# Performance work log

Hardware: AMD Instinct MI355X
Metric: run time of the kernel (lower is better)

## Reference

```python
import jax, jax.numpy as jnp
import numpy as np

D_MODEL = 192; D_INNER = 384; N_STATE = 16; D_CONV = 4; DT_RANK = 12; DEPTH = 24
PATCH = 16; STRIDE = 16; IMG = 128; EPS = 1e-5


def _ln(x, w, b):
    m = jnp.mean(x, -1, keepdims=True)
    v = jnp.mean((x - m) ** 2, -1, keepdims=True)
    return (x - m) * jax.lax.rsqrt(v + EPS) * w + b


def _mamba_dir(xz, cw, cb, xpw, dpw, dpb, Alog, Dv):
    # xz: (B, L, 2*d_inner); one direction of the bidirectional Mamba mixer
    xp, z = jnp.split(xz, 2, axis=-1)               # (B,L,di) each
    xc = jnp.transpose(xp, (0, 2, 1))               # (B,di,L)
    xc = jnp.pad(xc, ((0, 0), (0, 0), (D_CONV - 1, 0)))  # causal pad
    xc = jax.lax.conv_general_dilated(
        xc, cw, (1,), 'VALID',
        dimension_numbers=('NCH', 'OIH', 'NCH'),
        feature_group_count=D_INNER) + cb[None, :, None]
    u = jax.nn.silu(jnp.transpose(xc, (0, 2, 1)))   # (B,L,di)
    dbl = u @ xpw.T                                  # (B,L,dt_rank+2N)
    dt, Bm, Cm = jnp.split(dbl, [DT_RANK, DT_RANK + N_STATE], axis=-1)
    dt = jax.nn.softplus(dt @ dpw.T + dpb)           # (B,L,di)
    A = -jnp.exp(Alog)                               # (di,N)
    dA = jnp.exp(dt[..., None] * A)                  # (B,L,di,N)
    dBu = (dt * u)[..., None] * Bm[:, :, None, :]    # (B,L,di,N)

    def comb(c1, c2):
        a1, b1 = c1
        a2, b2 = c2
        return a1 * a2, a2 * b1 + b2

    _, h = jax.lax.associative_scan(comb, (dA, dBu), axis=1)
    y = jnp.einsum('bldn,bln->bld', h, Cm) + u * Dv
    return y * jax.nn.silu(z)


def _forward(x, patch_w, patch_b, ln_w, ln_b, in_w,
             cf_w, cf_b, xpf_w, dtf_w, dtf_b, Alog_f, D_f,
             cbk_w, cbk_b, xpb_w, dtb_w, dtb_b, Alog_b, D_b,
             out_w, nf_w, nf_b, head_w, head_b):
    B = x.shape[0]
    p = jax.lax.conv_general_dilated(
        x, patch_w, (STRIDE,) * 3, 'VALID',
        dimension_numbers=('NCDHW', 'OIDHW', 'NCDHW')) + patch_b[None, :, None, None, None]
    hidden = p.reshape(B, D_MODEL, -1).transpose(0, 2, 1)  # (B, L=512, D)
    residual = jnp.zeros_like(hidden)

    xs = (ln_w, ln_b, in_w, cf_w, cf_b, xpf_w, dtf_w, dtf_b, Alog_f, D_f,
          cbk_w, cbk_b, xpb_w, dtb_w, dtb_b, Alog_b, D_b, out_w)

    def step(carry, pl):
        hidden, residual = carry
        (lw, lb, iw, cfw, cfb, xpf, dwf, dbf, Af, Dfv,
         cbw, cbb, xpb, dwb, dbb, Ab, Dbv, ow) = pl
        residual = residual + hidden
        hn = _ln(residual, lw, lb)
        xz = hn @ iw.T                               # (B,L,2di)
        yf = _mamba_dir(xz, cfw, cfb, xpf, dwf, dbf, Af, Dfv)
        yb = jnp.flip(_mamba_dir(jnp.flip(xz, 1), cbw, cbb, xpb, dwb, dbb, Ab, Dbv), 1)
        hidden = (yf + yb) @ ow.T
        return (hidden, residual), None

    (hidden, residual), _ = jax.lax.scan(step, (hidden, residual), xs)
    final = _ln(residual + hidden, nf_w, nf_b)
    feat = final[:, -1, :]                           # final_pool_type='none' -> last token
    return feat @ head_w.T + head_b


def setup_inputs() -> dict:
    key = jax.random.key(0)
    ks = jax.random.split(key, 16)
    rn = lambda k, s, sc=0.02: jax.random.normal(k, s, jnp.float32) * sc
    d = {}
    d['x'] = jax.random.normal(ks[0], (1, 1, IMG, IMG, IMG), jnp.float32)
    d['patch_w'] = rn(ks[1], (D_MODEL, 1, PATCH, PATCH, PATCH), 0.05)
    d['patch_b'] = jnp.zeros((D_MODEL,), jnp.float32)
    d['ln_w'] = jnp.ones((DEPTH, D_MODEL), jnp.float32)
    d['ln_b'] = jnp.zeros((DEPTH, D_MODEL), jnp.float32)
    d['in_w'] = rn(ks[2], (DEPTH, 2 * D_INNER, D_MODEL))
    d['cf_w'] = rn(ks[3], (DEPTH, D_INNER, 1, D_CONV), 0.2)
    d['cf_b'] = jnp.zeros((DEPTH, D_INNER), jnp.float32)
    d['xpf_w'] = rn(ks[4], (DEPTH, DT_RANK + 2 * N_STATE, D_INNER))
    d['dtf_w'] = rn(ks[5], (DEPTH, D_INNER, DT_RANK), 0.1)
    d['dtf_b'] = jnp.full((DEPTH, D_INNER), -4.6, jnp.float32)  # softplus -> dt~0.01
    d['Alog_f'] = jnp.log(jnp.broadcast_to(jnp.arange(1, N_STATE + 1, dtype=jnp.float32), (DEPTH, D_INNER, N_STATE)))
    d['D_f'] = jnp.ones((DEPTH, D_INNER), jnp.float32)
    d['cbk_w'] = rn(ks[6], (DEPTH, D_INNER, 1, D_CONV), 0.2)
    d['cbk_b'] = jnp.zeros((DEPTH, D_INNER), jnp.float32)
    d['xpb_w'] = rn(ks[7], (DEPTH, DT_RANK + 2 * N_STATE, D_INNER))
    d['dtb_w'] = rn(ks[8], (DEPTH, D_INNER, DT_RANK), 0.1)
    d['dtb_b'] = jnp.full((DEPTH, D_INNER), -4.6, jnp.float32)
    d['Alog_b'] = jnp.log(jnp.broadcast_to(jnp.arange(1, N_STATE + 1, dtype=jnp.float32), (DEPTH, D_INNER, N_STATE)))
    d['D_b'] = jnp.ones((DEPTH, D_INNER), jnp.float32)
    d['out_w'] = rn(ks[9], (DEPTH, D_MODEL, D_INNER))
    d['nf_w'] = jnp.ones((D_MODEL,), jnp.float32)
    d['nf_b'] = jnp.zeros((D_MODEL,), jnp.float32)
    d['head_w'] = rn(ks[10], (2, D_MODEL))
    d['head_b'] = jnp.zeros((2,), jnp.float32)
    return d


def reference(x, patch_w, patch_b, ln_w, ln_b, in_w,
              cf_w, cf_b, xpf_w, dtf_w, dtf_b, Alog_f, D_f,
              cbk_w, cbk_b, xpb_w, dtb_w, dtb_b, Alog_b, D_b,
              out_w, nf_w, nf_b, head_w, head_b):
    return _forward(x, patch_w, patch_b, ln_w, ln_b, in_w,
                    cf_w, cf_b, xpf_w, dtf_w, dtf_b, Alog_f, D_f,
                    cbk_w, cbk_b, xpb_w, dtb_w, dtb_b, Alog_b, D_b,
                    out_w, nf_w, nf_b, head_w, head_b)
```

## Files before the change

kernel.cpp:

```cpp
#include <hip/hip_runtime.h>
#include <hip/hip_bf16.h>

#define D_MODEL 192
#define D_INNER 384
#define N_STATE 16
#define DT_RANK 12
#define DEPTH 24
#define SEQ 512
#define NCHUNK 8
#define CLEN 64
#define TS 68
#define AS 33
#define PART_STRIDE (SEQ * D_MODEL)
#define USTR (SEQ * D_INNER)
#define KSPLIT 16
#define NBLK 512

typedef __hip_bfloat16 bf16;
typedef unsigned short u16;

__device__ __forceinline__ float silu_f(float x) { return x / (1.f + __expf(-x)); }
__device__ __forceinline__ float softplus_f(float x) {
    return (x > 20.f) ? x : log1pf(__expf(x));
}
__device__ __forceinline__ float bf2f(unsigned u) {
    return __uint_as_float(u << 16);
}
__device__ __forceinline__ u16 f2bu(float f) {
    bf16 b = __float2bfloat16(f);
    return *reinterpret_cast<u16*>(&b);
}

__device__ __forceinline__ float aload(const float* p) {
    return __hip_atomic_load(p, __ATOMIC_RELAXED, __HIP_MEMORY_SCOPE_AGENT);
}
__device__ __forceinline__ void astore(float* p, float v) {
    __hip_atomic_store(p, v, __ATOMIC_RELAXED, __HIP_MEMORY_SCOPE_AGENT);
}
__device__ __forceinline__ float4 aload4(const float* p) {
    return make_float4(aload(p), aload(p + 1), aload(p + 2), aload(p + 3));
}
__device__ __forceinline__ void astore4(float* p, float4 v) {
    astore(p, v.x); astore(p + 1, v.y); astore(p + 2, v.z); astore(p + 3, v.w);
}

template<typename T> __device__ __forceinline__ float ld(const void* p, long i) {
    return ((const float*)p)[i];
}
template<> __device__ __forceinline__ float ld<bf16>(const void* p, long i) {
    return bf2f(((const u16*)p)[i]);
}
template<typename T> __device__ __forceinline__ float4 ld4(const void* p, long i) {
    return *(const float4*)((const float*)p + i);
}
template<> __device__ __forceinline__ float4 ld4<bf16>(const void* p, long i) {
    const ushort4 v = *(const ushort4*)((const u16*)p + i);
    return make_float4(bf2f(v.x), bf2f(v.y), bf2f(v.z), bf2f(v.w));
}
template<typename T> __device__ __forceinline__ void st(void* p, int i, float v) {
    ((float*)p)[i] = v;
}
template<> __device__ __forceinline__ void st<bf16>(void* p, int i, float v) {
    ((bf16*)p)[i] = __float2bfloat16(v);
}
__device__ __forceinline__ float dot4(const float4& a, const float4& b) {
    return a.x * b.x + a.y * b.y + a.z * b.z + a.w * b.w;
}
__device__ __forceinline__ void ld8b(const u16* p, float4& a, float4& b) {
    const uint4 u = *(const uint4*)p;
    a.x = bf2f(u.x & 0xffffu); a.y = bf2f(u.x >> 16);
    a.z = bf2f(u.y & 0xffffu); a.w = bf2f(u.y >> 16);
    b.x = bf2f(u.z & 0xffffu); b.y = bf2f(u.z >> 16);
    b.z = bf2f(u.w & 0xffffu); b.w = bf2f(u.w >> 16);
}
__device__ __forceinline__ float4 ld4b(const u16* p) {
    const uint2 u = *(const uint2*)p;
    return make_float4(bf2f(u.x & 0xffffu), bf2f(u.x >> 16),
                       bf2f(u.y & 0xffffu), bf2f(u.y >> 16));
}

__device__ __forceinline__ void gbar_full(unsigned* flags, unsigned* gen, unsigned target) {
    __syncthreads();
    const int bid = blockIdx.x, tid = threadIdx.x;
    if (tid == 0) {
        __threadfence();
        __hip_atomic_store(&flags[bid], target, __ATOMIC_RELAXED, __HIP_MEMORY_SCOPE_AGENT);
    }
    if (bid == 0) {
        int spins = 0;
        for (;;) {
            const unsigned va = __hip_atomic_load(&flags[tid], __ATOMIC_RELAXED, __HIP_MEMORY_SCOPE_AGENT);
            const unsigned vb = __hip_atomic_load(&flags[tid + 256], __ATOMIC_RELAXED, __HIP_MEMORY_SCOPE_AGENT);
            const bool ok = (va >= target) && (vb >= target);
            if (__syncthreads_and(ok)) break;
            if (++spins > (1 << 20)) break;
            __builtin_amdgcn_s_sleep(1);
        }
        if (tid == 0)
            __hip_atomic_store(gen, target, __ATOMIC_RELAXED, __HIP_MEMORY_SCOPE_AGENT);
    } else if (tid == 0) {
        int spins = 0;
        while (__hip_atomic_load(gen, __ATOMIC_RELAXED, __HIP_MEMORY_SCOPE_AGENT) < target) {
            if (++spins > (1 << 20)) break;
            __builtin_amdgcn_s_sleep(1);
        }
    }
    if (tid == 0) __threadfence();
    __syncthreads();
}

__device__ __forceinline__ void gbar_lite(unsigned* flags, unsigned* gen, unsigned target) {
    asm volatile("s_waitcnt vmcnt(0)" ::: "memory");
    __syncthreads();
    const int bid = blockIdx.x, tid = threadIdx.x;
    if (tid == 0)
        __hip_atomic_store(&flags[bid], target, __ATOMIC_RELAXED, __HIP_MEMORY_SCOPE_AGENT);
    if (bid == 0) {
        int spins = 0;
        for (;;) {
            const unsigned va = __hip_atomic_load(&flags[tid], __ATOMIC_RELAXED, __HIP_MEMORY_SCOPE_AGENT);
            const unsigned vb = __hip_atomic_load(&flags[tid + 256], __ATOMIC_RELAXED, __HIP_MEMORY_SCOPE_AGENT);
            const bool ok = (va >= target) && (vb >= target);
            if (__syncthreads_and(ok)) break;
            if (++spins > (1 << 20)) break;
            __builtin_amdgcn_s_sleep(1);
        }
        if (tid == 0)
            __hip_atomic_store(gen, target, __ATOMIC_RELAXED, __HIP_MEMORY_SCOPE_AGENT);
    } else if (tid == 0) {
        int spins = 0;
        while (__hip_atomic_load(gen, __ATOMIC_RELAXED, __HIP_MEMORY_SCOPE_AGENT) < target) {
            if (++spins > (1 << 20)) break;
            __builtin_amdgcn_s_sleep(1);
        }
    }
    __syncthreads();
}

__device__ void cvtB(const void* s, u16* d, long n, long g, long str, int isb) {
    if (isb) {
        const u16* p = (const u16*)s;
        for (long i = g * 4; i < n; i += str * 4) *(ushort4*)(d + i) = *(const ushort4*)(p + i);
    } else {
        const float* p = (const float*)s;
        for (long i = g * 4; i < n; i += str * 4) {
            const float4 v = *(const float4*)(p + i);
            ushort4 o; o.x = f2bu(v.x); o.y = f2bu(v.y); o.z = f2bu(v.z); o.w = f2bu(v.w);
            *(ushort4*)(d + i) = o;
        }
    }
}
__device__ void cvtF(const void* s, float* d, long n, long g, long str, int isb) {
    if (isb) {
        const u16* p = (const u16*)s;
        for (long i = g * 4; i < n; i += str * 4) {
            const ushort4 v = *(const ushort4*)(p + i);
            *(float4*)(d + i) = make_float4(bf2f(v.x), bf2f(v.y), bf2f(v.z), bf2f(v.w));
        }
    } else {
        const float* p = (const float*)s;
        for (long i = g * 4; i < n; i += str * 4) *(float4*)(d + i) = *(const float4*)(p + i);
    }
}
__device__ void cvtNA(const void* s, float* d, long n, long g, long str, int isb) {
    if (isb) {
        const u16* p = (const u16*)s;
        for (long i = g * 4; i < n; i += str * 4) {
            const ushort4 v = *(const ushort4*)(p + i);
            *(float4*)(d + i) = make_float4(-__expf(bf2f(v.x)), -__expf(bf2f(v.y)),
                                            -__expf(bf2f(v.z)), -__expf(bf2f(v.w)));
        }
    } else {
        const float* p = (const float*)s;
        for (long i = g * 4; i < n; i += str * 4) {
            const float4 v = *(const float4*)(p + i);
            *(float4*)(d + i) = make_float4(-__expf(v.x), -__expf(v.y), -__expf(v.z), -__expf(v.w));
        }
    }
}

template<typename T>
__device__ void final_phase(int tid, const float* res, const float* y, const void* ow,
                            const void* nw, const void* nb, const void* hw, const void* hb,
                            void* out, float* syf, float* f, float* red) {
    for (int i = tid; i < D_INNER; i += 256)
        syf[i] = aload(&y[(long)511 * D_INNER + i]) + aload(&y[(long)USTR + 511 * D_INNER + i]);
    __syncthreads();
    float v = 0.f;
    if (tid < D_MODEL) {
        float acc = 0.f;
        const long wrow = (long)(DEPTH - 1) * D_MODEL * D_INNER + (long)tid * D_INNER;
        for (int k = 0; k < D_INNER; k += 4)
            acc += dot4(ld4<T>(ow, wrow + k), *(const float4*)&syf[k]);
        v = aload(&res[511 * D_MODEL + tid]) + acc;
    }
    float s = v;
    #pragma unroll
    for (int o = 32; o > 0; o >>= 1) s += __shfl_down(s, o, 64);
    if ((tid & 63) == 0 && tid < D_MODEL) red[tid >> 6] = s;
    __syncthreads();
    const float mean = (red[0] + red[1] + red[2]) * (1.f / D_MODEL);
    const float d = (tid < D_MODEL) ? (v - mean) : 0.f;
    float s2 = d * d;
    #pragma unroll
    for (int o = 32; o > 0; o >>= 1) s2 += __shfl_down(s2, o, 64);
    if ((tid & 63) == 0 && tid < D_MODEL) red[3 + (tid >> 6)] = s2;
    __syncthreads();
    const float var = (red[3] + red[4] + red[5]) * (1.f / D_MODEL);
    if (tid < D_MODEL)
        f[tid] = d * rsqrtf(var + 1e-5f) * ld<T>(nw, tid) + ld<T>(nb, tid);
    __syncthreads();
    if (tid < 2) {
        float a2 = ld<T>(hb, tid);
        for (int c = 0; c < D_MODEL; ++c) a2 += f[c] * ld<T>(hw, tid * D_MODEL + c);
        st<T>(out, tid, a2);
    }
}

struct MegaArgs {
    const void *x, *pw, *pb, *lnw, *lnb, *inw, *cfw, *cfb, *xpfw, *dtfw, *dtfb, *Af, *Dfv;
    const void *cbw, *cbb, *xpbw, *dtbw, *dtbb, *Ab, *Dbv, *ow, *nfw, *nfb, *hw, *hb;
    void* out;
    unsigned* bar;
    float *hidC, *res0, *res1, *xz, *u, *dbl, *dt, *y, *chunkH, *chunkP;
    float *lnwF, *lnbF, *cbfF, *cbbF, *dtbfF, *dtbbF, *negAfF, *negAbF, *DfF, *DbF, *pbF;
    u16 *inwB, *owB, *xB, *pwB, *xpwfB, *xpwbB, *dtwfB, *dtwbB, *cwfB, *cwbB;
};

__global__ void init_kernel(unsigned* bar) {
    for (int i = threadIdx.x; i < 1024; i += 256) bar[i] = 0;
}

__global__ void __launch_bounds__(256, 2) mega_kernel(MegaArgs a) {
    __shared__ float smem[6144];
    const int bid = blockIdx.x;
    const int tid = threadIdx.x;
    unsigned* bflags = a.bar;
    unsigned* bgen = a.bar + 576;
    unsigned gen_ctr = 0;
    const int isb = (((const unsigned*)a.lnw)[0] != 0x3F800000u);

    {
        const long g = (long)bid * 256 + tid;
        const long str = (long)NBLK * 256;
        cvtB(a.inw,  a.inwB,  3538944, g, str, isb);
        cvtB(a.ow,   a.owB,   1769472, g, str, isb);
        cvtB(a.x,    a.xB,    2097152, g, str, isb);
        cvtB(a.pw,   a.pwB,    786432, g, str, isb);
        cvtB(a.xpfw, a.xpwfB,  405504, g, str, isb);
        cvtB(a.xpbw, a.xpwbB,  405504, g, str, isb);
        cvtB(a.dtfw, a.dtwfB,  110592, g, str, isb);
        cvtB(a.dtbw, a.dtwbB,  110592, g, str, isb);
        cvtB(a.cfw,  a.cwfB,    36864, g, str, isb);
        cvtB(a.cbw,  a.cwbB,    36864, g, str, isb);
        cvtF(a.lnw,  a.lnwF,     4608, g, str, isb);
        cvtF(a.lnb,  a.lnbF,     4608, g, str, isb);
        cvtF(a.cfb,  a.cbfF,     9216, g, str, isb);
        cvtF(a.cbb,  a.cbbF,     9216, g, str, isb);
        cvtF(a.dtfb, a.dtbfF,    9216, g, str, isb);
        cvtF(a.dtbb, a.dtbbF,    9216, g, str, isb);
        cvtF(a.pb,   a.pbF,       192, g, str, isb);
        cvtNA(a.Af,  a.negAfF,  147456, g, str, isb);
        cvtNA(a.Ab,  a.negAbF,  147456, g, str, isb);
        cvtF(a.Dfv,  a.DfF,      9216, g, str, isb);
        cvtF(a.Dbv,  a.DbF,      9216, g, str, isb);
    }
    gbar_full(bflags, bgen, ++gen_ctr);

    {
        float* As_ = smem;
        float* Ws  = smem + 1056;
        const int ty = tid >> 4, tx = tid & 15;
        for (int unit = bid; unit < 768; unit += NBLK) {
            const int mt = unit & 15, nt = (unit >> 4) % 3, ks = unit / 48;
            const int m0 = mt * 32, n0 = nt * 64, kk0 = ks * 256;
            float acc[2][4] = {};
            for (int kk = kk0; kk < kk0 + 256; kk += 32) {
                for (int e = tid; e < 1024; e += 256) {
                    const int m = e >> 5, k = e & 31;
                    const int kid = kk + k, t = m0 + m;
                    const int dz = kid >> 8, dy = (kid >> 4) & 15, dx = kid & 15;
                    const int pz = t >> 6, py = (t >> 3) & 7, px = t & 7;
                    As_[k * AS + m] = bf2f(a.xB[(long)(pz * 16 + dz) * 16384 + (py * 16 + dy) * 128 + (px * 16 + dx)]);
                }
                for (int e = tid; e < 2048; e += 256) {
                    const int n = e >> 5, k = e & 31;
                    Ws[k * TS + n] = bf2f(a.pwB[(long)(n0 + n) * 4096 + kk + k]);
                }
                __syncthreads();
                #pragma unroll 8
                for (int k = 0; k < 32; ++k) {
                    const float a0 = As_[k * AS + ty * 2];
                    const float a1 = As_[k * AS + ty * 2 + 1];
                    const float4 w4 = *(const float4*)&Ws[k * TS + tx * 4];
                    acc[0][0] += a0 * w4.x; acc[0][1] += a0 * w4.y;
                    acc[0][2] += a0 * w4.z; acc[0][3] += a0 * w4.w;
                    acc[1][0] += a1 * w4.x; acc[1][1] += a1 * w4.y;
                    acc[1][2] += a1 * w4.z; acc[1][3] += a1 * w4.w;
                }
                __syncthreads();
            }
            float* C = a.hidC + (long)ks * PART_STRIDE;
            #pragma unroll
            for (int i = 0; i < 2; ++i) {
                float4 o4 = make_float4(acc[i][0], acc[i][1], acc[i][2], acc[i][3]);
                if (ks == 0) {
                    o4.x += a.pbF[n0 + tx * 4 + 0];
                    o4.y += a.pbF[n0 + tx * 4 + 1];
                    o4.z += a.pbF[n0 + tx * 4 + 2];
                    o4.w += a.pbF[n0 + tx * 4 + 3];
                }
                astore4(&C[(m0 + ty * 2 + i) * D_MODEL + n0 + tx * 4], o4);
            }
        }
    }
    gbar_lite(bflags, bgen, ++gen_ctr);

    const int ch = tid >> 4, np = tid & 15;
    float* sU  = smem;
    float* sDT = smem + 1024;
    float* sBC = smem + 2048;
    float* sZ  = smem + 4096;
    float* sY  = smem + 5120;
    int dg = 0, chunk = 0, dir2 = 0;
    float Areg = 0.f, Dval = 0.f;

    for (int l = 0; l < DEPTH; ++l) {
        const int first = (l == 0);
        const float* resIn = (l & 1) ? a.res1 : a.res0;
        float* resOut      = (l & 1) ? a.res0 : a.res1;

        if (bid < 256) {
            float* sy  = smem;
            float* lnS = smem + 768;
            float* hnS = smem + 1152;
            const int t0 = bid * 2;
            if (!first) {
                for (int i = tid; i < 2 * D_INNER; i += 256) {
                    const int tt = i / D_INNER, d = i - tt * D_INNER;
                    const long o = (long)(t0 + tt) * D_INNER + d;
                    sy[i] = aload(&a.y[o]) + aload(&a.y[(long)USTR + o]);
                }
            }
            __syncthreads();
            if (tid < D_MODEL) {
                float accB[2];
                if (first) {
                    #pragma unroll
                    for (int tt = 0; tt < 2; ++tt) {
                        float s = 0.f;
                        #pragma unroll
                        for (int sp = 0; sp < KSPLIT; ++sp)
                            s += aload(&a.hidC[(long)sp * PART_STRIDE + (t0 + tt) * D_MODEL + tid]);
                        accB[tt] = s;
                    }
                } else {
                    accB[0] = accB[1] = 0.f;
                    const u16* wr = a.owB + (long)(l - 1) * D_MODEL * D_INNER + (long)tid * D_INNER;
                    for (int k = 0; k < D_INNER; k += 8) {
                        float4 va, vb;
                        ld8b(wr + k, va, vb);
                        accB[0] += dot4(va, *(const float4*)&sy[k]) + dot4(vb, *(const float4*)&sy[k + 4]);
                        accB[1] += dot4(va, *(const float4*)&sy[D_INNER + k]) + dot4(vb, *(const float4*)&sy[D_INNER + k + 4]);
                    }
                }
                #pragma unroll
                for (int tt = 0; tt < 2; ++tt) {
                    const float rv = accB[tt] + (first ? 0.f : aload(&resIn[(t0 + tt) * D_MODEL + tid]));
                    lnS[tt * D_MODEL + tid] = rv;
                    astore(&resOut[(t0 + tt) * D_MODEL + tid], rv);
                }
            }
            __syncthreads();
            {
                const int w = tid >> 6, lane = tid & 63;
                if (w < 2) {
                    const float v0 = lnS[w * D_MODEL + lane];
                    const float v1 = lnS[w * D_MODEL + lane + 64];
                    const float v2 = lnS[w * D_MODEL + lane + 128];
                    float s = v0 + v1 + v2;
                    #pragma unroll
                    for (int o = 32; o > 0; o >>= 1) s += __shfl_xor(s, o, 64);
                    const float mean = s * (1.f / D_MODEL);
                    const float d0 = v0 - mean, d1 = v1 - mean, d2 = v2 - mean;
                    float s2 = d0 * d0 + d1 * d1 + d2 * d2;
                    #pragma unroll
                    for (int o = 32; o > 0; o >>= 1) s2 += __shfl_xor(s2, o, 64);
                    const float rstd = rsqrtf(s2 * (1.f / D_MODEL) + 1e-5f);
                    hnS[w * D_MODEL + lane]       = d0 * rstd * a.lnwF[l * D_MODEL + lane]       + a.lnbF[l * D_MODEL + lane];
                    hnS[w * D_MODEL + lane + 64]  = d1 * rstd * a.lnwF[l * D_MODEL + lane + 64]  + a.lnbF[l * D_MODEL + lane + 64];
                    hnS[w * D_MODEL + lane + 128] = d2 * rstd * a.lnwF[l * D_MODEL + lane + 128] + a.lnbF[l * D_MODEL + lane + 128];
                }
            }
            __syncthreads();
            float accD[3][2] = {};
            const u16* w0 = a.inwB + (long)l * 2 * D_INNER * D_MODEL;
            for (int k = 0; k < D_MODEL; k += 8) {
                #pragma unroll
                for (int r = 0; r < 3; ++r) {
                    float4 va, vb;
                    ld8b(w0 + (long)(tid + r * 256) * D_MODEL + k, va, vb);
                    #pragma unroll
                    for (int tt = 0; tt < 2; ++tt) {
                        accD[r][tt] += dot4(va, *(const float4*)&hnS[tt * D_MODEL + k])
                                     + dot4(vb, *(const float4*)&hnS[tt * D_MODEL + k + 4]);
                    }
                }
            }
            #pragma unroll
            for (int r = 0; r < 3; ++r)
                #pragma unroll
                for (int tt = 0; tt < 2; ++tt)
                    astore(&a.xz[(long)(t0 + tt) * 2 * D_INNER + tid + r * 256], accD[r][tt]);
        }
        gbar_lite(bflags, bgen, ++gen_ctr);

        {
            float* su   = smem;
            float* dblP = smem + 768;
            float* dblS = smem + 960;
            const int dir = bid >> 8;
            const u16* cwB   = dir ? a.cwbB  : a.cwfB;
            const float* cbF = dir ? a.cbbF  : a.cbfF;
            const u16* xpwB  = dir ? a.xpwbB : a.xpwfB;
            const u16* dtwB  = dir ? a.dtwbB : a.dtwfB;
            const float* dtbF = dir ? a.dtbbF : a.dtbfF;
            const int t0 = (bid & 255) * 2;
            float* ub = a.u + (long)dir * USTR;
            for (int i = tid; i < 2 * D_INNER; i += 256) {
                const int tt = i / D_INNER, d = i - tt * D_INNER;
                const int t = t0 + tt;
                const float4 w4 = ld4b(cwB + (long)(l * D_INNER + d) * 4);
                const float cwk[4] = {w4.x, w4.y, w4.z, w4.w};
                float acc = cbF[l * D_INNER + d];
                #pragma unroll
                for (int k = 0; k < 4; ++k) {
                    const int ii = t + k - 3;
                    if (ii >= 0) {
                        const int src = dir ? (511 - ii) : ii;
                        acc += aload(&a.xz[(long)src * 2 * D_INNER + d]) * cwk[k];
                    }
                }
                const float uv = silu_f(acc);
                su[tt * D_INNER + d] = uv;
                astore(&ub[(long)t * D_INNER + d], uv);
            }
            __syncthreads();
            if (tid < 176) {
                const int half = tid / 88;
                const int r = tid - half * 88;
                const int tt = r / 44, out = r - tt * 44;
                const u16* wr = xpwB + (long)(l * 44 + out) * D_INNER;
                const int k0 = half * 192;
                float acc = 0.f;
                for (int k = k0; k < k0 + 192; k += 8) {
                    float4 va, vb;
                    ld8b(wr + k, va, vb);
                    acc += dot4(va, *(const float4*)&su[tt * D_INNER + k])
                         + dot4(vb, *(const float4*)&su[tt * D_INNER + k + 4]);
                }
                dblP[half * 96 + tt * 48 + out] = acc;
            }
            __syncthreads();
            if (tid < 88) {
                const int tt = tid / 44, out = tid - tt * 44;
                const float s = dblP[tt * 48 + out] + dblP[96 + tt * 48 + out];
                dblS[tt * 48 + out] = s;
                astore(&a.dbl[(long)dir * SEQ * 44 + (long)(t0 + tt) * 44 + out], s);
            }
            __syncthreads();
            float* dtp = a.dt + (long)dir * USTR;
            for (int i = tid; i < 2 * D_INNER; i += 256) {
                const int tt = i / D_INNER, d = i - tt * D_INNER;
                const u16* wr = dtwB + (long)(l * D_INNER + d) * DT_RANK;
                const float4 wa = ld4b(wr), wb2 = ld4b(wr + 4), wc = ld4b(wr + 8);
                const float* ds = &dblS[tt * 48];
                float acc = dtbF[l * D_INNER + d]
                    + wa.x * ds[0] + wa.y * ds[1] + wa.z * ds[2] + wa.w * ds[3]
                    + wb2.x * ds[4] + wb2.y * ds[5] + wb2.z * ds[6] + wb2.w * ds[7]
                    + wc.x * ds[8] + wc.y * ds[9] + wc.z * ds[10] + wc.w * ds[11];
                astore(&dtp[(long)(t0 + tt) * D_INNER + d], softplus_f(acc));
            }
        }
        gbar_lite(bflags, bgen, ++gen_ctr);

        if (bid < 384) {
            dg = bid % 24; chunk = (bid / 24) & 7; dir2 = bid / 192;
            const int d0 = dg * 16, d = d0 + ch;
            const int t0s = chunk * CLEN;
            const float* ub  = a.u  + (long)dir2 * USTR;
            const float* dtp = a.dt + (long)dir2 * USTR;
            const float* db  = a.dbl + (long)dir2 * SEQ * 44;
            {
                const int t = tid >> 2, dl4 = (tid & 3) * 4;
                const int tg = t0s + t;
                const long base = (long)tg * D_INNER + d0 + dl4;
                *(float4*)&sU[t * 16 + dl4]  = aload4(&ub[base]);
                *(float4*)&sDT[t * 16 + dl4] = aload4(&dtp[base]);
                const int out_l = dir2 ? (511 - tg) : tg;
                *(float4*)&sZ[t * 16 + dl4] = aload4(&a.xz[(long)out_l * 2 * D_INNER + D_INNER + d0 + dl4]);
            }
            for (int i = tid; i < 512; i += 256) {
                const int t = i >> 3, j4 = (i & 7) * 4;
                *(float4*)&sBC[t * 32 + j4] = aload4(&db[(long)(t0s + t) * 44 + DT_RANK + j4]);
            }
            const float* negA = dir2 ? a.negAbF : a.negAfF;
            Areg = negA[(long)(l * D_INNER + d) * N_STATE + np];
            Dval = (dir2 ? a.DbF : a.DfF)[l * D_INNER + d];
            __syncthreads();
            float h = 0.f, dts = 0.f;
            for (int t = 0; t < CLEN; ++t) {
                const float dtv = sDT[t * 16 + ch];
                h = __expf(dtv * Areg) * h + (dtv * sU[t * 16 + ch]) * sBC[t * 32 + np];
                dts += dtv;
            }
            const long cb = ((long)(dir2 * NCHUNK + chunk) * D_INNER + d) * N_STATE + np;
            astore(&a.chunkH[cb], h);
            astore(&a.chunkP[cb], __expf(Areg * dts));
        }
        gbar_lite(bflags, bgen, ++gen_ctr);

        if (bid < 384) {
            const int d0 = dg * 16, d = d0 + ch;
            const int t0s = chunk * CLEN;
            float hs[NCHUNK - 1], ps[NCHUNK - 1];
            #pragma unroll
            for (int c = 0; c < NCHUNK - 1; ++c) {
                if (c < chunk) {
                    const long cb = ((long)(dir2 * NCHUNK + c) * D_INNER + d) * N_STATE + np;
                    hs[c] = aload(&a.chunkH[cb]);
                    ps[c] = aload(&a.chunkP[cb]);
                }
            }
            float h = 0.f;
            #pragma unroll
            for (int c = 0; c < NCHUNK - 1; ++c)
                if (c < chunk) h = ps[c] * h + hs[c];
            for (int t = 0; t < CLEN; ++t) {
                const float dtv = sDT[t * 16 + ch];
                const float uv = sU[t * 16 + ch];
                h = __expf(dtv * Areg) * h + (dtv * uv) * sBC[t * 32 + np];
                float part = h * sBC[t * 32 + 16 + np];
                part += __shfl_xor(part, 1, 64);
                part += __shfl_xor(part, 2, 64);
                part += __shfl_xor(part, 4, 64);
                part += __shfl_xor(part, 8, 64);
                if (np == 0)
                    sY[t * 16 + ch] = (part + uv * Dval) * silu_f(sZ[t * 16 + ch]);
            }
            __syncthreads();
            {
                const int t = tid >> 2, dl4 = (tid & 3) * 4;
                const int tg = t0s + t;
                const int out_l = dir2 ? (511 - tg) : tg;
                float* yb = a.y + (long)dir2 * USTR;
                astore4(&yb[(long)out_l * D_INNER + d0 + dl4], *(float4*)&sY[t * 16 + dl4]);
            }
        }
        gbar_lite(bflags, bgen, ++gen_ctr);
    }

    if (bid == 0) {
        float* syf = smem;
        float* f   = smem + 384;
        float* red = smem + 576;
        if (isb) final_phase<bf16>(tid, a.res0, a.y, a.ow, a.nfw, a.nfb, a.hw, a.hb, a.out, syf, f, red);
        else     final_phase<float>(tid, a.res0, a.y, a.ow, a.nfw, a.nfb, a.hw, a.hb, a.out, syf, f, red);
    }
}

extern "C" void kernel_launch(void* const* d_in, const int* in_sizes, int n_in,
                              void* d_out, int out_size, void* d_ws, size_t ws_size,
                              hipStream_t stream) {
    (void)in_sizes; (void)n_in; (void)out_size; (void)ws_size;
    const void* x    = d_in[0];
    const void* pw   = d_in[1];
    const void* pb   = d_in[2];
    const void* lnw  = d_in[3];
    const void* lnb  = d_in[4];
    const void* inw  = d_in[5];
    const void* cfw  = d_in[6];
    const void* cfb  = d_in[7];
    const void* xpfw = d_in[8];
    const void* dtfw = d_in[9];
    const void* dtfb = d_in[10];
    const void* Af   = d_in[11];
    const void* Dfv  = d_in[12];
    const void* cbw  = d_in[13];
    const void* cbb  = d_in[14];
    const void* xpbw = d_in[15];
    const void* dtbw = d_in[16];
    const void* dtbb = d_in[17];
    const void* Ab   = d_in[18];
    const void* Dbv  = d_in[19];
    const void* ow   = d_in[20];
    const void* nfw  = d_in[21];
    const void* nfb  = d_in[22];
    const void* hw   = d_in[23];
    const void* hb   = d_in[24];

    unsigned* bar = (unsigned*)d_ws;
    float* w = (float*)((char*)d_ws + 4096);
    float* hidC   = w;  w += KSPLIT * PART_STRIDE;
    float* res0   = w;  w += PART_STRIDE;
    float* res1   = w;  w += PART_STRIDE;
    float* xz     = w;  w += SEQ * 2 * D_INNER;
    float* u      = w;  w += 2 * USTR;
    float* dbl    = w;  w += 2 * SEQ * 44;
    float* dt     = w;  w += 2 * USTR;
    float* y      = w;  w += 2 * USTR;
    float* chunkH = w;  w += 2 * NCHUNK * D_INNER * N_STATE;
    float* chunkP = w;  w += 2 * NCHUNK * D_INNER * N_STATE;
    float* lnwF = w;  w += 4608;
    float* lnbF = w;  w += 4608;
    float* cbfF = w;  w += 9216;
    float* cbbF = w;  w += 9216;
    float* dtbfF = w; w += 9216;
    float* dtbbF = w; w += 9216;
    float* negAfF = w; w += 147456;
    float* negAbF = w; w += 147456;
    float* DfF = w;   w += 9216;
    float* DbF = w;   w += 9216;
    float* pbF = w;   w += 192;
    u16* b = (u16*)w;
    u16* inwB  = b;  b += 3538944;
    u16* owB   = b;  b += 1769472;
    u16* xB    = b;  b += 2097152;
    u16* pwB   = b;  b += 786432;
    u16* xpwfB = b;  b += 405504;
    u16* xpwbB = b;  b += 405504;
    u16* dtwfB = b;  b += 110592;
    u16* dtwbB = b;  b += 110592;
    u16* cwfB  = b;  b += 36864;
    u16* cwbB  = b;  b += 36864;

    MegaArgs ma;
    ma.x = x; ma.pw = pw; ma.pb = pb; ma.lnw = lnw; ma.lnb = lnb; ma.inw = inw;
    ma.cfw = cfw; ma.cfb = cfb; ma.xpfw = xpfw; ma.dtfw = dtfw; ma.dtfb = dtfb;
    ma.Af = Af; ma.Dfv = Dfv; ma.cbw = cbw; ma.cbb = cbb; ma.xpbw = xpbw;
    ma.dtbw = dtbw; ma.dtbb = dtbb; ma.Ab = Ab; ma.Dbv = Dbv; ma.ow = ow;
    ma.nfw = nfw; ma.nfb = nfb; ma.hw = hw; ma.hb = hb; ma.out = d_out;
    ma.bar = bar;
    ma.hidC = hidC; ma.res0 = res0; ma.res1 = res1; ma.xz = xz; ma.u = u;
    ma.dbl = dbl; ma.dt = dt; ma.y = y; ma.chunkH = chunkH; ma.chunkP = chunkP;
    ma.lnwF = lnwF; ma.lnbF = lnbF; ma.cbfF = cbfF; ma.cbbF = cbbF;
    ma.dtbfF = dtbfF; ma.dtbbF = dtbbF; ma.negAfF = negAfF; ma.negAbF = negAbF;
    ma.DfF = DfF; ma.DbF = DbF; ma.pbF = pbF;
    ma.inwB = inwB; ma.owB = owB; ma.xB = xB; ma.pwB = pwB;
    ma.xpwfB = xpwfB; ma.xpwbB = xpwbB; ma.dtwfB = dtwfB; ma.dtwbB = dtwbB;
    ma.cwfB = cwfB; ma.cwbB = cwbB;

    init_kernel<<<1, 256, 0, stream>>>(bar);
    mega_kernel<<<NBLK, 256, 0, stream>>>(ma);
}
```

Baseline: 2.123 ms.

## Pad barrier flags, tree-broadcast release, and replace scan barrier with per-chunk flags

The grid barrier now gives each block's flag its own padded slot, so flags no longer share cache lines. Release goes through a two-level fan-out: 16 relay blocks copy the generation and the other blocks poll their own relay slot instead of all spinning on one word. The global barrier between the chunk-local scan and the carry-in pass is replaced by per-chunk ready flags, so each chunk waits only on the earlier chunks it depends on. Atomic loads and stores are widened to 64-bit pairs, and the conv and dt-projection loops handle two channels per thread to halve the number of memory operations. The trade-offs are a larger workspace, more bookkeeping, and dependence on relaxed 64-bit atomics and spin flags for correctness.

```diff
diff --git a/kernel.cpp b/kernel.cpp
--- a/kernel.cpp
+++ b/kernel.cpp
@@ -15,9 +15,11 @@
 #define USTR (SEQ * D_INNER)
 #define KSPLIT 16
 #define NBLK 512
+#define FSTR 32
 
 typedef __hip_bfloat16 bf16;
 typedef unsigned short u16;
+typedef unsigned long long u64;
 
 __device__ __forceinline__ float silu_f(float x) { return x / (1.f + __expf(-x)); }
 __device__ __forceinline__ float softplus_f(float x) {
@@ -37,11 +39,26 @@
 __device__ __forceinline__ void astore(float* p, float v) {
     __hip_atomic_store(p, v, __ATOMIC_RELAXED, __HIP_MEMORY_SCOPE_AGENT);
 }
-__device__ __forceinline__ float4 aload4(const float* p) {
-    return make_float4(aload(p), aload(p + 1), aload(p + 2), aload(p + 3));
-}
-__device__ __forceinline__ void astore4(float* p, float4 v) {
-    astore(p, v.x); astore(p + 1, v.y); astore(p + 2, v.z); astore(p + 3, v.w);
+__device__ __forceinline__ unsigned aloadu(const unsigned* p) {
+    return __hip_atomic_load(p, __ATOMIC_RELAXED, __HIP_MEMORY_SCOPE_AGENT);
+}
+__device__ __forceinline__ void astoreu(unsigned* p, unsigned v) {
+    __hip_atomic_store(p, v, __ATOMIC_RELAXED, __HIP_MEMORY_SCOPE_AGENT);
+}
+__device__ __forceinline__ float2 aload2(const float* p) {
+    const u64 v = __hip_atomic_load((const u64*)p, __ATOMIC_RELAXED, __HIP_MEMORY_SCOPE_AGENT);
+    return make_float2(__uint_as_float((unsigned)v), __uint_as_float((unsigned)(v >> 32)));
+}
+__device__ __forceinline__ void astore2(float* p, float x, float y) {
+    const u64 v = (u64)__float_as_uint(x) | ((u64)__float_as_uint(y) << 32);
+    __hip_atomic_store((u64*)p, v, __ATOMIC_RELAXED, __HIP_MEMORY_SCOPE_AGENT);
+}
+__device__ __forceinline__ float4 aload4v(const float* p) {
+    const float2 a = aload2(p), b = aload2(p + 2);
+    return make_float4(a.x, a.y, b.x, b.y);
+}
+__device__ __forceinline__ void astore4v(float* p, float4 v) {
+    astore2(p, v.x, v.y); astore2(p + 2, v.z, v.w);
 }
 
 template<typename T> __device__ __forceinline__ float ld(const void* p, long i) {
@@ -79,61 +96,48 @@
                        bf2f(u.y & 0xffffu), bf2f(u.y >> 16));
 }
 
-__device__ __forceinline__ void gbar_full(unsigned* flags, unsigned* gen, unsigned target) {
+__device__ __forceinline__ void gbar(unsigned* bar, unsigned target, bool fence) {
+    asm volatile("s_waitcnt vmcnt(0)" ::: "memory");
     __syncthreads();
     const int bid = blockIdx.x, tid = threadIdx.x;
+    unsigned* gen0 = bar + 512 * FSTR;
     if (tid == 0) {
-        __threadfence();
-        __hip_atomic_store(&flags[bid], target, __ATOMIC_RELAXED, __HIP_MEMORY_SCOPE_AGENT);
+        if (fence) __threadfence();
+        astoreu(&bar[bid * FSTR], target);
     }
     if (bid == 0) {
         int spins = 0;
         for (;;) {
-            const unsigned va = __hip_atomic_load(&flags[tid], __ATOMIC_RELAXED, __HIP_MEMORY_SCOPE_AGENT);
-            const unsigned vb = __hip_atomic_load(&flags[tid + 256], __ATOMIC_RELAXED, __HIP_MEMORY_SCOPE_AGENT);
+            const unsigned va = aloadu(&bar[tid * FSTR]);
+            const unsigned vb = aloadu(&bar[(tid + 256) * FSTR]);
             const bool ok = (va >= target) && (vb >= target);
             if (__syncthreads_and(ok)) break;
             if (++spins > (1 << 20)) break;
             __builtin_amdgcn_s_sleep(1);
         }
-        if (tid == 0)
-            __hip_atomic_store(gen, target, __ATOMIC_RELAXED, __HIP_MEMORY_SCOPE_AGENT);
+        if (tid == 0) astoreu(gen0, target);
     } else if (tid == 0) {
         int spins = 0;
-        while (__hip_atomic_load(gen, __ATOMIC_RELAXED, __HIP_MEMORY_SCOPE_AGENT) < target) {
-            if (++spins > (1 << 20)) break;
-            __builtin_amdgcn_s_sleep(1);
-        }
-    }
-    if (tid == 0) __threadfence();
-    __syncthreads();
-}
-
-__device__ __forceinline__ void gbar_lite(unsigned* flags, unsigned* gen, unsigned target) {
-    asm volatile("s_waitcnt vmcnt(0)" ::: "memory");
-    __syncthreads();
-    const int bid = blockIdx.x, tid = threadIdx.x;
-    if (tid == 0)
-        __hip_atomic_store(&flags[bid], target, __ATOMIC_RELAXED, __HIP_MEMORY_SCOPE_AGENT);
-    if (bid == 0) {
-        int spins = 0;
-        for (;;) {
-            const unsigned va = __hip_atomic_load(&flags[tid], __ATOMIC_RELAXED, __HIP_MEMORY_SCOPE_AGENT);
-            const unsigned vb = __hip_atomic_load(&flags[tid + 256], __ATOMIC_RELAXED, __HIP_MEMORY_SCOPE_AGENT);
-            const bool ok = (va >= target) && (vb >= target);
-            if (__syncthreads_and(ok)) break;
-            if (++spins > (1 << 20)) break;
-            __builtin_amdgcn_s_sleep(1);
-        }
-        if (tid == 0)
-            __hip_atomic_store(gen, target, __ATOMIC_RELAXED, __HIP_MEMORY_SCOPE_AGENT);
-    } else if (tid == 0) {
-        int spins = 0;
-        while (__hip_atomic_load(gen, __ATOMIC_RELAXED, __HIP_MEMORY_SCOPE_AGENT) < target) {
-            if (++spins > (1 << 20)) break;
-            __builtin_amdgcn_s_sleep(1);
-        }
-    }
+        if (bid < 16) {
+            while (aloadu(gen0) < target) {
+                if (++spins > (1 << 20)) break;
+                __builtin_amdgcn_s_sleep(2);
+            }
+            astoreu(&gen0[bid * FSTR], target);
+        } else if (bid < 32) {
+            while (aloadu(gen0) < target) {
+                if (++spins > (1 << 20)) break;
+                __builtin_amdgcn_s_sleep(2);
+            }
+        } else {
+            unsigned* rl = &gen0[(bid >> 5) * FSTR];
+            while (aloadu(rl) < target) {
+                if (++spins > (1 << 20)) break;
+                __builtin_amdgcn_s_sleep(2);
+            }
+        }
+    }
+    if (fence && tid == 0) __threadfence();
     __syncthreads();
 }
 
@@ -228,15 +232,16 @@
 };
 
 __global__ void init_kernel(unsigned* bar) {
-    for (int i = threadIdx.x; i < 1024; i += 256) bar[i] = 0;
+    const int i = blockIdx.x * 256 + threadIdx.x;
+    ((uint4*)bar)[i] = make_uint4(0, 0, 0, 0);
 }
 
 __global__ void __launch_bounds__(256, 2) mega_kernel(MegaArgs a) {
     __shared__ float smem[6144];
     const int bid = blockIdx.x;
     const int tid = threadIdx.x;
-    unsigned* bflags = a.bar;
-    unsigned* bgen = a.bar + 576;
+    unsigned* bar = a.bar;
+    unsigned* scanR = a.bar + 528 * FSTR;
     unsigned gen_ctr = 0;
     const int isb = (((const unsigned*)a.lnw)[0] != 0x3F800000u);
 
@@ -265,7 +270,7 @@
         cvtF(a.Dfv,  a.DfF,      9216, g, str, isb);
         cvtF(a.Dbv,  a.DbF,      9216, g, str, isb);
     }
-    gbar_full(bflags, bgen, ++gen_ctr);
+    gbar(bar, ++gen_ctr, true);
 
     {
         float* As_ = smem;
@@ -310,11 +315,11 @@
                     o4.z += a.pbF[n0 + tx * 4 + 2];
                     o4.w += a.pbF[n0 + tx * 4 + 3];
                 }
-                astore4(&C[(m0 + ty * 2 + i) * D_MODEL + n0 + tx * 4], o4);
-            }
-        }
-    }
-    gbar_lite(bflags, bgen, ++gen_ctr);
+                astore4v(&C[(m0 + ty * 2 + i) * D_MODEL + n0 + tx * 4], o4);
+            }
+        }
+    }
+    gbar(bar, ++gen_ctr, false);
 
     const int ch = tid >> 4, np = tid & 15;
     float* sU  = smem;
@@ -322,8 +327,6 @@
     float* sBC = smem + 2048;
     float* sZ  = smem + 4096;
     float* sY  = smem + 5120;
-    int dg = 0, chunk = 0, dir2 = 0;
-    float Areg = 0.f, Dval = 0.f;
 
     for (int l = 0; l < DEPTH; ++l) {
         const int first = (l == 0);
@@ -336,10 +339,13 @@
             float* hnS = smem + 1152;
             const int t0 = bid * 2;
             if (!first) {
-                for (int i = tid; i < 2 * D_INNER; i += 256) {
-                    const int tt = i / D_INNER, d = i - tt * D_INNER;
-                    const long o = (long)(t0 + tt) * D_INNER + d;
-                    sy[i] = aload(&a.y[o]) + aload(&a.y[(long)USTR + o]);
+                for (int j = tid; j < 384; j += 256) {
+                    const int tt = j / 192, d2 = (j - tt * 192) * 2;
+                    const long o = (long)(t0 + tt) * D_INNER + d2;
+                    const float2 v1 = aload2(&a.y[o]);
+                    const float2 v2 = aload2(&a.y[(long)USTR + o]);
+                    sy[tt * D_INNER + d2]     = v1.x + v2.x;
+                    sy[tt * D_INNER + d2 + 1] = v1.y + v2.y;
                 }
             }
             __syncthreads();
@@ -413,7 +419,7 @@
                 for (int tt = 0; tt < 2; ++tt)
                     astore(&a.xz[(long)(t0 + tt) * 2 * D_INNER + tid + r * 256], accD[r][tt]);
         }
-        gbar_lite(bflags, bgen, ++gen_ctr);
+        gbar(bar, ++gen_ctr, false);
 
         {
             float* su   = smem;
@@ -427,23 +433,29 @@
             const float* dtbF = dir ? a.dtbbF : a.dtbfF;
             const int t0 = (bid & 255) * 2;
             float* ub = a.u + (long)dir * USTR;
-            for (int i = tid; i < 2 * D_INNER; i += 256) {
-                const int tt = i / D_INNER, d = i - tt * D_INNER;
+            for (int j = tid; j < 384; j += 256) {
+                const int tt = j / 192, d2 = (j - tt * 192) * 2;
                 const int t = t0 + tt;
-                const float4 w4 = ld4b(cwB + (long)(l * D_INNER + d) * 4);
-                const float cwk[4] = {w4.x, w4.y, w4.z, w4.w};
-                float acc = cbF[l * D_INNER + d];
+                float4 wa, wb;
+                ld8b(cwB + (long)(l * D_INNER + d2) * 4, wa, wb);
+                const float cw0[4] = {wa.x, wa.y, wa.z, wa.w};
+                const float cw1[4] = {wb.x, wb.y, wb.z, wb.w};
+                float acc0 = cbF[l * D_INNER + d2];
+                float acc1 = cbF[l * D_INNER + d2 + 1];
                 #pragma unroll
                 for (int k = 0; k < 4; ++k) {
                     const int ii = t + k - 3;
                     if (ii >= 0) {
                         const int src = dir ? (511 - ii) : ii;
-                        acc += aload(&a.xz[(long)src * 2 * D_INNER + d]) * cwk[k];
+                        const float2 xv = aload2(&a.xz[(long)src * 2 * D_INNER + d2]);
+                        acc0 += xv.x * cw0[k];
+                        acc1 += xv.y * cw1[k];
                     }
                 }
-                const float uv = silu_f(acc);
-                su[tt * D_INNER + d] = uv;
-                astore(&ub[(long)t * D_INNER + d], uv);
+                const float u0 = silu_f(acc0), u1 = silu_f(acc1);
+                su[tt * D_INNER + d2] = u0;
+                su[tt * D_INNER + d2 + 1] = u1;
+                astore2(&ub[(long)t * D_INNER + d2], u0, u1);
             }
             __syncthreads();
             if (tid < 176) {
@@ -470,22 +482,29 @@
             }
             __syncthreads();
             float* dtp = a.dt + (long)dir * USTR;
-            for (int i = tid; i < 2 * D_INNER; i += 256) {
-                const int tt = i / D_INNER, d = i - tt * D_INNER;
-                const u16* wr = dtwB + (long)(l * D_INNER + d) * DT_RANK;
-                const float4 wa = ld4b(wr), wb2 = ld4b(wr + 4), wc = ld4b(wr + 8);
+            for (int j = tid; j < 384; j += 256) {
+                const int tt = j / 192, d2 = (j - tt * 192) * 2;
+                const u16* wr = dtwB + (long)(l * D_INNER + d2) * DT_RANK;
+                float4 A0, B0; ld8b(wr, A0, B0);
+                const float4 C0 = ld4b(wr + 8);
+                float4 A1, B1; ld8b(wr + 12, A1, B1);
+                const float4 C1 = ld4b(wr + 20);
                 const float* ds = &dblS[tt * 48];
-                float acc = dtbF[l * D_INNER + d]
-                    + wa.x * ds[0] + wa.y * ds[1] + wa.z * ds[2] + wa.w * ds[3]
-                    + wb2.x * ds[4] + wb2.y * ds[5] + wb2.z * ds[6] + wb2.w * ds[7]
-                    + wc.x * ds[8] + wc.y * ds[9] + wc.z * ds[10] + wc.w * ds[11];
-                astore(&dtp[(long)(t0 + tt) * D_INNER + d], softplus_f(acc));
-            }
-        }
-        gbar_lite(bflags, bgen, ++gen_ctr);
+                const float4 ds0 = *(const float4*)ds;
+                const float4 ds1 = *(const float4*)(ds + 4);
+                const float4 ds2 = *(const float4*)(ds + 8);
+                const float acc0 = dtbF[l * D_INNER + d2]
+                    + dot4(A0, ds0) + dot4(B0, ds1) + dot4(C0, ds2);
+                const float acc1 = dtbF[l * D_INNER + d2 + 1]
+                    + dot4(A1, ds0) + dot4(B1, ds1) + dot4(C1, ds2);
+                astore2(&dtp[(long)(t0 + tt) * D_INNER + d2],
+                        softplus_f(acc0), softplus_f(acc1));
+            }
+        }
+        gbar(bar, ++gen_ctr, false);
 
         if (bid < 384) {
-            dg = bid % 24; chunk = (bid / 24) & 7; dir2 = bid / 192;
+            const int dg = bid % 24, chunk = (bid / 24) & 7, dir2 = bid / 192;
             const int d0 = dg * 16, d = d0 + ch;
             const int t0s = chunk * CLEN;
             const float* ub  = a.u  + (long)dir2 * USTR;
@@ -495,18 +514,18 @@
                 const int t = tid >> 2, dl4 = (tid & 3) * 4;
                 const int tg = t0s + t;
                 const long base = (long)tg * D_INNER + d0 + dl4;
-                *(float4*)&sU[t * 16 + dl4]  = aload4(&ub[base]);
-                *(float4*)&sDT[t * 16 + dl4] = aload4(&dtp[base]);
+                *(float4*)&sU[t * 16 + dl4]  = aload4v(&ub[base]);
+                *(float4*)&sDT[t * 16 + dl4] = aload4v(&dtp[base]);
                 const int out_l = dir2 ? (511 - tg) : tg;
-                *(float4*)&sZ[t * 16 + dl4] = aload4(&a.xz[(long)out_l * 2 * D_INNER + D_INNER + d0 + dl4]);
+                *(float4*)&sZ[t * 16 + dl4] = aload4v(&a.xz[(long)out_l * 2 * D_INNER + D_INNER + d0 + dl4]);
             }
             for (int i = tid; i < 512; i += 256) {
                 const int t = i >> 3, j4 = (i & 7) * 4;
-                *(float4*)&sBC[t * 32 + j4] = aload4(&db[(long)(t0s + t) * 44 + DT_RANK + j4]);
+                *(float4*)&sBC[t * 32 + j4] = aload4v(&db[(long)(t0s + t) * 44 + DT_RANK + j4]);
             }
             const float* negA = dir2 ? a.negAbF : a.negAfF;
-            Areg = negA[(long)(l * D_INNER + d) * N_STATE + np];
-            Dval = (dir2 ? a.DbF : a.DfF)[l * D_INNER + d];
+            const float Areg = negA[(long)(l * D_INNER + d) * N_STATE + np];
+            const float Dval = (dir2 ? a.DbF : a.DfF)[l * D_INNER + d];
             __syncthreads();
             float h = 0.f, dts = 0.f;
             for (int t = 0; t < CLEN; ++t) {
@@ -517,25 +536,33 @@
             const long cb = ((long)(dir2 * NCHUNK + chunk) * D_INNER + d) * N_STATE + np;
             astore(&a.chunkH[cb], h);
             astore(&a.chunkP[cb], __expf(Areg * dts));
-        }
-        gbar_lite(bflags, bgen, ++gen_ctr);
-
-        if (bid < 384) {
-            const int d0 = dg * 16, d = d0 + ch;
-            const int t0s = chunk * CLEN;
+            asm volatile("s_waitcnt vmcnt(0)" ::: "memory");
+            __syncthreads();
+            if (tid == 0)
+                astoreu(&scanR[((dir2 * NCHUNK + chunk) * 24 + dg) * FSTR], (unsigned)(l + 1));
+            if (tid < chunk) {
+                unsigned* fl = &scanR[((dir2 * NCHUNK + tid) * 24 + dg) * FSTR];
+                int spins = 0;
+                while (aloadu(fl) < (unsigned)(l + 1)) {
+                    if (++spins > (1 << 20)) break;
+                    __builtin_amdgcn_s_sleep(1);
+                }
+            }
+            __syncthreads();
             float hs[NCHUNK - 1], ps[NCHUNK - 1];
             #pragma unroll
             for (int c = 0; c < NCHUNK - 1; ++c) {
                 if (c < chunk) {
-                    const long cb = ((long)(dir2 * NCHUNK + c) * D_INNER + d) * N_STATE + np;
-                    hs[c] = aload(&a.chunkH[cb]);
-                    ps[c] = aload(&a.chunkP[cb]);
-                }
-            }
-            float h = 0.f;
+                    const long cbb = ((long)(dir2 * NCHUNK + c) * D_INNER + d) * N_STATE + np;
+                    hs[c] = aload(&a.chunkH[cbb]);
+                    ps[c] = aload(&a.chunkP[cbb]);
+                }
+            }
+            float h0 = 0.f;
             #pragma unroll
             for (int c = 0; c < NCHUNK - 1; ++c)
-                if (c < chunk) h = ps[c] * h + hs[c];
+                if (c < chunk) h0 = ps[c] * h0 + hs[c];
+            h = h0;
             for (int t = 0; t < CLEN; ++t) {
                 const float dtv = sDT[t * 16 + ch];
                 const float uv = sU[t * 16 + ch];
@@ -554,10 +581,10 @@
                 const int tg = t0s + t;
                 const int out_l = dir2 ? (511 - tg) : tg;
                 float* yb = a.y + (long)dir2 * USTR;
-                astore4(&yb[(long)out_l * D_INNER + d0 + dl4], *(float4*)&sY[t * 16 + dl4]);
-            }
-        }
-        gbar_lite(bflags, bgen, ++gen_ctr);
+                astore4v(&yb[(long)out_l * D_INNER + d0 + dl4], *(float4*)&sY[t * 16 + dl4]);
+            }
+        }
+        gbar(bar, ++gen_ctr, false);
     }
 
     if (bid == 0) {
@@ -600,7 +627,7 @@
     const void* hb   = d_in[24];
 
     unsigned* bar = (unsigned*)d_ws;
-    float* w = (float*)((char*)d_ws + 4096);
+    float* w = (float*)((char*)d_ws + 131072);
     float* hidC   = w;  w += KSPLIT * PART_STRIDE;
     float* res0   = w;  w += PART_STRIDE;
     float* res1   = w;  w += PART_STRIDE;
@@ -650,6 +677,6 @@
     ma.xpwfB = xpwfB; ma.xpwbB = xpwbB; ma.dtwfB = dtwfB; ma.dtwbB = dtwbB;
     ma.cwfB = cwfB; ma.cwbB = cwbB;
 
-    init_kernel<<<1, 256, 0, stream>>>(bar);
+    init_kernel<<<32, 256, 0, stream>>>(bar);
     mega_kernel<<<NBLK, 256, 0, stream>>>(ma);
 }
```

Measured after the change: 2.049 ms. 3.5% less time.
